# Kernel tuning notes

Measured on AMD Instinct MI355X. Metric: run time of the kernel, lower is better.

Reference implementation:

```python
import jax, jax.numpy as jnp
import numpy as np

# ---- static ragged feature layout (from CTGAN metadata) ----
NUM_CLUSTERS = [10, 8, 10, 5, 10, 10, 7, 10, 10, 10]          # per numerical feature
NUM_CATEGORIES = [2, 5, 10, 3, 50, 4, 2, 8, 100, 6, 2, 3, 12, 5, 2, 30, 4, 9, 2, 7]
TAU = 0.2        # GumbelSoftmax temperature (teras default)
BN_EPS = 1e-3    # keras BatchNormalization default epsilon
LATENT_DIM = 128
BATCH = 65536

_seg, _alpha = [], []
_gid = 0
for c in NUM_CLUSTERS:
    _seg.append(_gid); _alpha.append(True); _gid += 1        # alpha scalar (tanh), own segment
    _seg += [_gid] * c; _alpha += [False] * c; _gid += 1     # beta cluster group (gumbel softmax)
for k in NUM_CATEGORIES:
    _seg += [_gid] * k; _alpha += [False] * k; _gid += 1     # categorical group (gumbel softmax)
SEG = jnp.asarray(np.array(_seg, dtype=np.int32))
ALPHA_MASK = jnp.asarray(np.array(_alpha, dtype=bool))
N_SEG = _gid
DATA_DIM = len(_seg)  # 366


def setup_inputs() -> dict:
    key = jax.random.key(0)
    ks = jax.random.split(key, 8)
    z = jax.random.normal(ks[0], (BATCH, LATENT_DIM), dtype=jnp.float32)
    # pre-sampled standard Gumbel noise for the gumbel-softmax groups
    u = jax.random.uniform(ks[1], (BATCH, DATA_DIM), dtype=jnp.float32, minval=1e-6, maxval=1.0 - 1e-6)
    g = -jnp.log(-jnp.log(u))
    def w(k, fi, fo):
        return jax.random.normal(k, (fi, fo), dtype=jnp.float32) * (1.0 / np.sqrt(fi))
    return {
        "z": z, "g": g,
        "W1": w(ks[2], LATENT_DIM, 256), "b1": jnp.zeros((256,), jnp.float32),
        "gamma1": jnp.ones((256,), jnp.float32), "beta1": jnp.zeros((256,), jnp.float32),
        "W2": w(ks[3], LATENT_DIM + 256, 256), "b2": jnp.zeros((256,), jnp.float32),
        "gamma2": jnp.ones((256,), jnp.float32), "beta2": jnp.zeros((256,), jnp.float32),
        "Wout": w(ks[4], LATENT_DIM + 512, DATA_DIM), "bout": jnp.zeros((DATA_DIM,), jnp.float32),
    }


def _bn_relu(h, gamma, beta):
    # training-mode batch norm (batch statistics), as used while training CTGAN
    mu = jnp.mean(h, axis=0)
    var = jnp.var(h, axis=0)
    return jax.nn.relu((h - mu) * jax.lax.rsqrt(var + BN_EPS) * gamma + beta)


def reference(z, g, W1, b1, gamma1, beta1, W2, b2, gamma2, beta2, Wout, bout):
    # CTGAN residual generator layers: out = concat([relu(bn(dense(x))), x])
    h1 = jnp.concatenate([_bn_relu(z @ W1 + b1, gamma1, beta1), z], axis=1)    # [B, 384]
    h2 = jnp.concatenate([_bn_relu(h1 @ W2 + b2, gamma2, beta2), h1], axis=1)  # [B, 640]
    logits = h2 @ Wout + bout                                                  # [B, 366]

    # ragged per-group gumbel-softmax: segment-wise stable softmax over columns
    zt = ((logits + g) / TAU).T                                   # [D, B]
    m = jax.ops.segment_max(zt, SEG, num_segments=N_SEG)          # [S, B]
    e = jnp.exp(zt - m[SEG])
    s = jax.ops.segment_sum(e, SEG, num_segments=N_SEG)
    soft = (e / s[SEG]).T                                         # [B, D]
    # alpha columns: tanh of raw logits; all other columns: group softmax
    return jnp.where(ALPHA_MASK[None, :], jnp.tanh(logits), soft)
```

## Files before the change

kernel.cpp:

```cpp
#include <hip/hip_runtime.h>

typedef _Float16 half_t;
typedef _Float16 half4 __attribute__((ext_vector_type(4)));
typedef _Float16 half8 __attribute__((ext_vector_type(8)));
typedef float f32x4 __attribute__((ext_vector_type(4)));

#define AS1 __attribute__((address_space(1)))
#define AS3 __attribute__((address_space(3)))

static constexpr int NBATCH = 65536;

__global__ __launch_bounds__(256) void k_cvtz(const float* __restrict__ z,
                                              half_t* __restrict__ dst) {
  size_t i = (size_t)blockIdx.x * 256 + threadIdx.x;
  int row = (int)(i >> 4), c8 = (int)(i & 15) << 3;
  const float* s = z + (size_t)row * 128 + c8;
  float4 v0 = *(const float4*)s;
  float4 v1 = *(const float4*)(s + 4);
  half8 h;
  h[0]=(half_t)v0.x; h[1]=(half_t)v0.y; h[2]=(half_t)v0.z; h[3]=(half_t)v0.w;
  h[4]=(half_t)v1.x; h[5]=(half_t)v1.y; h[6]=(half_t)v1.z; h[7]=(half_t)v1.w;
  *(half8*)(dst + (size_t)row * 640 + c8) = h;
}

__global__ __launch_bounds__(256) void k_transpose(const float* __restrict__ W,
                                                   half_t* __restrict__ Wt,
                                                   int K, int N, int total) {
  int i = blockIdx.x * 256 + threadIdx.x;
  if (i >= total) return;
  int n = i / K;
  int k = i - n * K;
  float v = (n < N) ? W[k * N + n] : 0.f;
  Wt[i] = (half_t)v;
}

template<bool STATS, bool F16OUT>
__global__ __launch_bounds__(256) void k_gemm(
    const half_t* __restrict__ A, int lda, int K,
    const half_t* __restrict__ Bt,
    const float* __restrict__ bias,
    half_t* __restrict__ o16, float* __restrict__ o32, int ldo, int ncreal,
    float* __restrict__ ps, float* __restrict__ pq) {
  __shared__ __align__(16) char smem[32768];
  half_t* Asm = (half_t*)smem;
  half_t* Bsm = (half_t*)(smem + 16384);
  const int tid  = threadIdx.x;
  const int lane = tid & 63;
  const int w    = tid >> 6;
  const int wr   = w >> 1, wc = w & 1;
  const int ml   = lane & 15, g = lane >> 4;
  const int brow = blockIdx.x * 128;
  const int bcol = blockIdx.y * 128;
  const int sr  = lane >> 3;
  const int scg = (lane & 7) ^ sr;

  f32x4 acc[4][4];
#pragma unroll
  for (int i = 0; i < 4; i++)
#pragma unroll
    for (int j = 0; j < 4; j++) acc[i][j] = (f32x4){0.f, 0.f, 0.f, 0.f};

  const half_t* Abase = A  + (size_t)brow * lda;
  const half_t* Bbase = Bt + (size_t)bcol * K;

  for (int k0 = 0; k0 < K; k0 += 64) {
    if (k0) __syncthreads();
#pragma unroll
    for (int it = 0; it < 4; it++) {
      int q = it * 4 + w;
      int r = q * 8 + sr;
      const half_t* ga = Abase + (size_t)r * lda + k0 + scg * 8;
      const half_t* gb = Bbase + (size_t)r * K   + k0 + scg * 8;
      __builtin_amdgcn_global_load_lds((AS1 const void*)ga, (AS3 void*)(Asm + q * 512), 16, 0, 0);
      __builtin_amdgcn_global_load_lds((AS1 const void*)gb, (AS3 void*)(Bsm + q * 512), 16, 0, 0);
    }
    __syncthreads();
#pragma unroll
    for (int kk = 0; kk < 64; kk += 16) {
      int k  = kk + g * 4;
      int cs = k >> 3;
      int ko = (k & 7) * 2;
      half4 af[4], bf[4];
#pragma unroll
      for (int fm = 0; fm < 4; fm++) {
        int row = wr * 64 + fm * 16 + ml;
        af[fm] = *(const half4*)((const char*)Asm + row * 128 + ((cs ^ (row & 7)) << 4) + ko);
      }
#pragma unroll
      for (int fn = 0; fn < 4; fn++) {
        int row = wc * 64 + fn * 16 + ml;
        bf[fn] = *(const half4*)((const char*)Bsm + row * 128 + ((cs ^ (row & 7)) << 4) + ko);
      }
#pragma unroll
      for (int fm = 0; fm < 4; fm++)
#pragma unroll
        for (int fn = 0; fn < 4; fn++)
          acc[fm][fn] = __builtin_amdgcn_mfma_f32_16x16x16f16(af[fm], bf[fn], acc[fm][fn], 0, 0, 0);
    }
  }
  __syncthreads();

#pragma unroll
  for (int fn = 0; fn < 4; fn++) {
    int col  = wc * 64 + fn * 16 + ml;
    int gcol = bcol + col;
    float bz = (gcol < ncreal) ? bias[gcol] : 0.f;
    float s = 0.f, q = 0.f;
#pragma unroll
    for (int fm = 0; fm < 4; fm++)
#pragma unroll
      for (int rr = 0; rr < 4; rr++) {
        float v = acc[fm][fn][rr] + bz;
        acc[fm][fn][rr] = v;
        if (STATS) { s += v; q += v * v; }
      }
    if (STATS) {
      s += __shfl_xor(s, 16, 64); s += __shfl_xor(s, 32, 64);
      q += __shfl_xor(q, 16, 64); q += __shfl_xor(q, 32, 64);
      if (g == 0) {
        ps[(size_t)gcol * 1024 + blockIdx.x * 2 + wr] = s;
        pq[(size_t)gcol * 1024 + blockIdx.x * 2 + wr] = q;
      }
    }
  }

  if (F16OUT) {
    half_t* so = (half_t*)smem;
#pragma unroll
    for (int fn = 0; fn < 4; fn++)
#pragma unroll
      for (int fm = 0; fm < 4; fm++)
#pragma unroll
        for (int rr = 0; rr < 4; rr++)
          so[(wr * 64 + fm * 16 + g * 4 + rr) * 128 + wc * 64 + fn * 16 + ml] =
              (half_t)acc[fm][fn][rr];
    __syncthreads();
#pragma unroll
    for (int it = 0; it < 8; it++) {
      int r = it * 16 + (tid >> 4);
      int c = (tid & 15) * 8;
      *(half8*)(o16 + (size_t)(brow + r) * ldo + bcol + c) = *(const half8*)&so[r * 128 + c];
    }
  } else {
    float* so = (float*)smem;
    for (int h = 0; h < 2; h++) {
      if (wr == h) {
#pragma unroll
        for (int fn = 0; fn < 4; fn++)
#pragma unroll
          for (int fm = 0; fm < 4; fm++)
#pragma unroll
            for (int rr = 0; rr < 4; rr++)
              so[(fm * 16 + g * 4 + rr) * 128 + wc * 64 + fn * 16 + ml] = acc[fm][fn][rr];
      }
      __syncthreads();
      int r0 = h * 64;
      for (int i = tid; i < 64 * 64; i += 256) {
        int r  = i >> 6;
        int c2 = (i & 63) * 2;
        int gc = bcol + c2;
        if (gc < ncreal)
          *(float2*)(o32 + (size_t)(brow + r0 + r) * ldo + gc) = *(const float2*)&so[r * 128 + c2];
      }
      __syncthreads();
    }
  }
}

__global__ __launch_bounds__(256) void k_bnfinal(
    const float* __restrict__ ps, const float* __restrict__ pq,
    const float* __restrict__ gamma, const float* __restrict__ beta,
    float* __restrict__ sc, float* __restrict__ sh) {
  int c = blockIdx.x, t = threadIdx.x;
  float s = 0.f, q = 0.f;
#pragma unroll
  for (int i = 0; i < 4; i++) {
    s += ps[(size_t)c * 1024 + t + i * 256];
    q += pq[(size_t)c * 1024 + t + i * 256];
  }
#pragma unroll
  for (int o = 1; o < 64; o <<= 1) { s += __shfl_xor(s, o, 64); q += __shfl_xor(q, o, 64); }
  __shared__ float ss[4], qq[4];
  if ((t & 63) == 0) { ss[t >> 6] = s; qq[t >> 6] = q; }
  __syncthreads();
  if (t == 0) {
    s = ss[0] + ss[1] + ss[2] + ss[3];
    q = qq[0] + qq[1] + qq[2] + qq[3];
    float mu   = s * (1.f / NBATCH);
    float var  = fmaxf(q * (1.f / NBATCH) - mu * mu, 0.f);
    float rstd = rsqrtf(var + 1e-3f);
    float a = gamma[c] * rstd;
    sc[c] = a;
    sh[c] = beta[c] - mu * a;
  }
}

__global__ __launch_bounds__(256) void k_bnrelu(half_t* __restrict__ p,
                                                const float* __restrict__ sc,
                                                const float* __restrict__ sh) {
  size_t i = (size_t)blockIdx.x * 256 + threadIdx.x;
  int row = (int)(i >> 5), c8 = (int)(i & 31) << 3;
  half_t* a = p + (size_t)row * 640 + c8;
  half8 v = *(const half8*)a;
  half8 o;
#pragma unroll
  for (int j = 0; j < 8; j++)
    o[j] = (half_t)fmaxf(fmaf((float)v[j], sc[c8 + j], sh[c8 + j]), 0.f);
  *(half8*)a = o;
}

template<int L>
__device__ __forceinline__ void seg_rt(float* __restrict__ zr, int S) {
  float v[L];
#pragma unroll
  for (int j = 0; j < L; j++) v[j] = zr[S + j];
  float m0 = -1e30f, m1 = -1e30f, m2 = -1e30f, m3 = -1e30f;
#pragma unroll
  for (int j = 0; j < L; j++) {
    if ((j & 3) == 0) m0 = fmaxf(m0, v[j]);
    else if ((j & 3) == 1) m1 = fmaxf(m1, v[j]);
    else if ((j & 3) == 2) m2 = fmaxf(m2, v[j]);
    else m3 = fmaxf(m3, v[j]);
  }
  const float m = fmaxf(fmaxf(m0, m1), fmaxf(m2, m3));
  float s0 = 0.f, s1 = 0.f, s2 = 0.f, s3 = 0.f;
#pragma unroll
  for (int j = 0; j < L; j++) {
    float e = __expf(v[j] - m);
    v[j] = e;
    if ((j & 3) == 0) s0 += e;
    else if ((j & 3) == 1) s1 += e;
    else if ((j & 3) == 2) s2 += e;
    else s3 += e;
  }
  const float inv = 1.0f / ((s0 + s1) + (s2 + s3));
#pragma unroll
  for (int j = 0; j < L; j++) zr[S + j] = v[j] * inv;
}

template<int L>
__device__ __forceinline__ void seg_pad(float* __restrict__ zr, int S, int Lr) {
  float v[L];
#pragma unroll
  for (int j = 0; j < L; j++) v[j] = (j < Lr) ? zr[S + j] : -1e30f;
  float m = -1e30f;
#pragma unroll
  for (int j = 0; j < L; j++) m = fmaxf(m, v[j]);
  float s = 0.f;
#pragma unroll
  for (int j = 0; j < L; j++) {
    float e = __expf(v[j] - m);
    v[j] = e;
    s += e;
  }
  const float inv = 1.0f / s;
#pragma unroll
  for (int j = 0; j < L; j++)
    if (j < Lr) zr[S + j] = v[j] * inv;
}

template<int S, int L>
__device__ __forceinline__ void seg_split(float* __restrict__ zr, int par) {
  constexpr int H = L / 2;
  const int base = S + par * H;
  float v[H];
#pragma unroll
  for (int j = 0; j < H; j++) v[j] = zr[base + j];
  float m = -1e30f;
#pragma unroll
  for (int j = 0; j < H; j++) m = fmaxf(m, v[j]);
  m = fmaxf(m, __shfl_xor(m, 1, 64));
  float s = 0.f;
#pragma unroll
  for (int j = 0; j < H; j++) {
    float e = __expf(v[j] - m);
    v[j] = e;
    s += e;
  }
  s += __shfl_xor(s, 1, 64);
  const float inv = 1.0f / s;
#pragma unroll
  for (int j = 0; j < H; j++) zr[base + j] = v[j] * inv;
}

template<int H>
__device__ __forceinline__ void seg_quad(float* __restrict__ zr, int base, int n) {
  float v[H];
#pragma unroll
  for (int j = 0; j < H; j++) v[j] = (j < n) ? zr[base + j] : -1e30f;
  float m = -1e30f;
#pragma unroll
  for (int j = 0; j < H; j++) m = fmaxf(m, v[j]);
  m = fmaxf(m, __shfl_xor(m, 1, 64));
  m = fmaxf(m, __shfl_xor(m, 2, 64));
  float s = 0.f;
#pragma unroll
  for (int j = 0; j < H; j++) {
    float e = __expf(v[j] - m);
    v[j] = e;
    s += e;
  }
  s += __shfl_xor(s, 1, 64);
  s += __shfl_xor(s, 2, 64);
  const float inv = 1.0f / s;
#pragma unroll
  for (int j = 0; j < H; j++)
    if (j < n) zr[base + j] = v[j] * inv;
}

__device__ __forceinline__ bool is_alpha(int c) {
  const unsigned long long AM0 =
      (1ull << 0) | (1ull << 11) | (1ull << 20) | (1ull << 31) | (1ull << 37) |
      (1ull << 48) | (1ull << 59);
  const unsigned long long AM1 = (1ull << 3) | (1ull << 14) | (1ull << 25);
  if (c >= 90) return false;
  return (((c < 64) ? (AM0 >> c) : (AM1 >> (c - 64))) & 1ull) != 0ull;
}

__global__ __launch_bounds__(512, 2) void k_softmax(const float* __restrict__ g,
                                                    float* __restrict__ out) {
  __shared__ float zb[32][373];
  const int tid = threadIdx.x;
  const size_t gbase = (size_t)blockIdx.x * 32 * 366;
  for (int i2 = tid; i2 < 32 * 183; i2 += 512) {
    int e0 = i2 * 2;
    int r = e0 / 366;
    int c = e0 - r * 366;
    float2 lg = *(const float2*)(out + gbase + e0);
    float2 gg = *(const float2*)(g + gbase + e0);
    zb[r][c]     = is_alpha(c)     ? tanhf(lg.x) : (lg.x + gg.x) * 5.0f;
    zb[r][c + 1] = is_alpha(c + 1) ? tanhf(lg.y) : (lg.y + gg.y) * 5.0f;
  }
  __syncthreads();
  {
    const int lane = tid & 63;
    const int w    = tid >> 6;
    const int par  = lane & 1;
    if (w < 4) {
      const int quad = lane & 3;
      float* zr = &zb[(w & 1) * 16 + (lane >> 2)][0];
      if (w < 2) {
        seg_quad<25>(zr, 184 + quad * 25, 25);
      } else {
        seg_quad<13>(zr, 120 + quad * 13 - (quad >> 1) * (quad & 1), 13 - (quad >> 1));
        seg_rt<10>(zr, par ? 68 : 1);
      }
    } else {
      float* zr = &zb[lane >> 1][0];
      switch (w) {
        case 4: seg_split<314, 30>(zr, par);
                seg_rt<7>(zr, par ? 359 : 60);
                seg_rt<2>(zr, par ? 174 : 100);
                seg_rt<2>(zr, par ? 312 : 290); break;
        case 5: seg_rt<10>(zr, par ? 90 : 38);
                seg_rt<10>(zr, par ? 107 : 49);
                seg_pad<2>(zr, par ? 357 : 0, par ? 2 : 0); break;
        case 6: seg_pad<12>(zr, par ? 348 : 295, par ? 9 : 12);
                seg_pad<6>(zr, par ? 284 : 32, par ? 6 : 5);
                seg_rt<5>(zr, par ? 307 : 102); break;
        default: seg_rt<10>(zr, par ? 79 : 21);
                 seg_rt<8>(zr, par ? 176 : 12);
                 seg_rt<4>(zr, par ? 344 : 170);
                 seg_rt<3>(zr, par ? 292 : 117); break;
      }
    }
  }
  __syncthreads();
  for (int i2 = tid; i2 < 32 * 183; i2 += 512) {
    int e0 = i2 * 2;
    int r = e0 / 366;
    int c = e0 - r * 366;
    float2 o;
    o.x = zb[r][c];
    o.y = zb[r][c + 1];
    *(float2*)(out + gbase + e0) = o;
  }
}

extern "C" void kernel_launch(void* const* d_in, const int* in_sizes, int n_in,
                              void* d_out, int out_size, void* d_ws, size_t ws_size,
                              hipStream_t stream) {
  const float* z      = (const float*)d_in[0];
  const float* g      = (const float*)d_in[1];
  const float* W1     = (const float*)d_in[2];
  const float* b1     = (const float*)d_in[3];
  const float* gamma1 = (const float*)d_in[4];
  const float* beta1  = (const float*)d_in[5];
  const float* W2     = (const float*)d_in[6];
  const float* b2     = (const float*)d_in[7];
  const float* gamma2 = (const float*)d_in[8];
  const float* beta2  = (const float*)d_in[9];
  const float* Wout   = (const float*)d_in[10];
  const float* bout   = (const float*)d_in[11];
  float* out = (float*)d_out;
  char* ws = (char*)d_ws;

  size_t off = 0;
  half_t* act = (half_t*)(ws + off); off += (size_t)NBATCH * 640 * 2;
  half_t* W1t = (half_t*)(ws + off); off += (size_t)256 * 128 * 2;
  half_t* W2t = (half_t*)(ws + off); off += (size_t)256 * 384 * 2;
  half_t* Wot = (half_t*)(ws + off); off += (size_t)384 * 640 * 2;
  float*  ps  = (float*)(ws + off);  off += (size_t)256 * 1024 * 4;
  float*  pq  = (float*)(ws + off);  off += (size_t)256 * 1024 * 4;
  float*  sc1 = (float*)(ws + off);  off += 256 * 4;
  float*  sh1 = (float*)(ws + off);  off += 256 * 4;
  float*  sc2 = (float*)(ws + off);  off += 256 * 4;
  float*  sh2 = (float*)(ws + off);  off += 256 * 4;
  (void)ws_size; (void)in_sizes; (void)n_in; (void)out_size;

  k_cvtz<<<4096, 256, 0, stream>>>(z, act + 512);
  k_transpose<<<(256 * 128 + 255) / 256, 256, 0, stream>>>(W1, W1t, 128, 256, 256 * 128);
  k_transpose<<<(256 * 384 + 255) / 256, 256, 0, stream>>>(W2, W2t, 384, 256, 256 * 384);
  k_transpose<<<(384 * 640 + 255) / 256, 256, 0, stream>>>(Wout, Wot, 640, 366, 384 * 640);

  k_gemm<true, true><<<dim3(512, 2), 256, 0, stream>>>(
      act + 512, 640, 128, W1t, b1, act + 256, nullptr, 640, 256, ps, pq);
  k_bnfinal<<<256, 256, 0, stream>>>(ps, pq, gamma1, beta1, sc1, sh1);
  k_bnrelu<<<8192, 256, 0, stream>>>(act + 256, sc1, sh1);

  k_gemm<true, true><<<dim3(512, 2), 256, 0, stream>>>(
      act + 256, 640, 384, W2t, b2, act + 0, nullptr, 640, 256, ps, pq);
  k_bnfinal<<<256, 256, 0, stream>>>(ps, pq, gamma2, beta2, sc2, sh2);
  k_bnrelu<<<8192, 256, 0, stream>>>(act + 0, sc2, sh2);

  k_gemm<false, false><<<dim3(512, 3), 256, 0, stream>>>(
      act, 640, 640, Wot, bout, nullptr, out, 366, 366, nullptr, nullptr);

  k_softmax<<<NBATCH / 32, 512, 0, stream>>>(g, out);
}
```

Baseline: 215.1 us.

## Double-buffer GEMM LDS tiles and switch to 16x16x32 f16 MFMA

The GEMM mainloop now keeps two LDS stages, 64KB in total. The next K-tile is loaded with global_load_lds while the current one is computed, using a partial vmcnt wait and raw barriers. The inner loop also uses the gfx950 16x16x32 f16 MFMA with half8 fragments, which halves the number of MFMA instructions and LDS reads. The larger LDS footprint can lower occupancy to one block per CU. The hand-written waitcnt and barrier sequence depends on the exact count of outstanding loads.

```diff
diff --git a/kernel.cpp b/kernel.cpp
--- a/kernel.cpp
+++ b/kernel.cpp
@@ -41,9 +41,7 @@
     const float* __restrict__ bias,
     half_t* __restrict__ o16, float* __restrict__ o32, int ldo, int ncreal,
     float* __restrict__ ps, float* __restrict__ pq) {
-  __shared__ __align__(16) char smem[32768];
-  half_t* Asm = (half_t*)smem;
-  half_t* Bsm = (half_t*)(smem + 16384);
+  __shared__ __align__(16) char smem[65536];
   const int tid  = threadIdx.x;
   const int lane = tid & 63;
   const int w    = tid >> 6;
@@ -62,42 +60,60 @@
 
   const half_t* Abase = A  + (size_t)brow * lda;
   const half_t* Bbase = Bt + (size_t)bcol * K;
-
-  for (int k0 = 0; k0 < K; k0 += 64) {
-    if (k0) __syncthreads();
+  const int nt = K >> 6;
+
+  auto stage = [&](int t, int p) {
+    half_t* As = (half_t*)(smem + p * 32768);
+    half_t* Bs = (half_t*)(smem + p * 32768 + 16384);
+    const int k0 = t * 64;
 #pragma unroll
     for (int it = 0; it < 4; it++) {
       int q = it * 4 + w;
       int r = q * 8 + sr;
-      const half_t* ga = Abase + (size_t)r * lda + k0 + scg * 8;
-      const half_t* gb = Bbase + (size_t)r * K   + k0 + scg * 8;
-      __builtin_amdgcn_global_load_lds((AS1 const void*)ga, (AS3 void*)(Asm + q * 512), 16, 0, 0);
-      __builtin_amdgcn_global_load_lds((AS1 const void*)gb, (AS3 void*)(Bsm + q * 512), 16, 0, 0);
-    }
-    __syncthreads();
-#pragma unroll
-    for (int kk = 0; kk < 64; kk += 16) {
-      int k  = kk + g * 4;
-      int cs = k >> 3;
-      int ko = (k & 7) * 2;
-      half4 af[4], bf[4];
+      __builtin_amdgcn_global_load_lds(
+          (AS1 const void*)(Abase + (size_t)r * lda + k0 + scg * 8),
+          (AS3 void*)(As + q * 512), 16, 0, 0);
+      __builtin_amdgcn_global_load_lds(
+          (AS1 const void*)(Bbase + (size_t)r * K + k0 + scg * 8),
+          (AS3 void*)(Bs + q * 512), 16, 0, 0);
+    }
+  };
+  auto compute = [&](int p) {
+    const char* As = (const char*)smem + p * 32768;
+    const char* Bs = (const char*)smem + p * 32768 + 16384;
+#pragma unroll
+    for (int t2 = 0; t2 < 2; t2++) {
+      const int c4 = t2 * 4 + g;
+      half8 af[4], bf[4];
 #pragma unroll
       for (int fm = 0; fm < 4; fm++) {
         int row = wr * 64 + fm * 16 + ml;
-        af[fm] = *(const half4*)((const char*)Asm + row * 128 + ((cs ^ (row & 7)) << 4) + ko);
+        af[fm] = *(const half8*)(As + row * 128 + ((c4 ^ (row & 7)) << 4));
       }
 #pragma unroll
       for (int fn = 0; fn < 4; fn++) {
         int row = wc * 64 + fn * 16 + ml;
-        bf[fn] = *(const half4*)((const char*)Bsm + row * 128 + ((cs ^ (row & 7)) << 4) + ko);
+        bf[fn] = *(const half8*)(Bs + row * 128 + ((c4 ^ (row & 7)) << 4));
       }
 #pragma unroll
       for (int fm = 0; fm < 4; fm++)
 #pragma unroll
         for (int fn = 0; fn < 4; fn++)
-          acc[fm][fn] = __builtin_amdgcn_mfma_f32_16x16x16f16(af[fm], bf[fn], acc[fm][fn], 0, 0, 0);
-    }
-  }
+          acc[fm][fn] = __builtin_amdgcn_mfma_f32_16x16x32_f16(af[fm], bf[fn], acc[fm][fn], 0, 0, 0);
+    }
+  };
+
+  stage(0, 0);
+  int p = 0;
+  for (int t = 0; t < nt - 1; t++) {
+    stage(t + 1, p ^ 1);
+    asm volatile("s_waitcnt vmcnt(8)\ns_barrier" ::: "memory");
+    compute(p);
+    asm volatile("s_barrier" ::: "memory");
+    p ^= 1;
+  }
+  asm volatile("s_waitcnt vmcnt(0)\ns_barrier" ::: "memory");
+  compute(p);
   __syncthreads();
 
 #pragma unroll
```

Result: faster. 207.1 us (-3.7%).
